# Optimization experiments

Measured on AMD Instinct MI355X. Metric: run time of the kernel, lower is better.

Reference implementation:

```python
import jax, jax.numpy as jnp
import numpy as np

DIM = 384
DEPTH = 4
HEADS = 6
DIM_HEAD = 64
INNER = HEADS * DIM_HEAD  # 384
MLP = 1536
B, N = 4, 2048


def setup_inputs() -> dict:
    key = jax.random.key(0)
    ks = jax.random.split(key, 7)
    s = 0.02
    x = jax.random.normal(ks[0], (B, N, DIM), dtype=jnp.float32)
    Wqkv = jax.random.normal(ks[1], (DEPTH, DIM, 3 * INNER), dtype=jnp.float32) * s
    Wout = jax.random.normal(ks[2], (DEPTH, INNER, DIM), dtype=jnp.float32) * s
    W1 = jax.random.normal(ks[3], (DEPTH, DIM, MLP), dtype=jnp.float32) * s
    b1 = jax.random.normal(ks[4], (DEPTH, MLP), dtype=jnp.float32) * s
    W2 = jax.random.normal(ks[5], (DEPTH, MLP, DIM), dtype=jnp.float32) * s
    b2 = jax.random.normal(ks[6], (DEPTH, DIM), dtype=jnp.float32) * s
    return {"x": x, "Wqkv": Wqkv, "Wout": Wout, "W1": W1, "b1": b1, "W2": W2, "b2": b2}


def _attention(x, Wqkv_l, Wout_l):
    scale = DIM_HEAD ** (-0.5)
    qkv = jnp.einsum('bnd,de->bne', x, Wqkv_l)  # [B,N,3*INNER]
    q, k, v = jnp.split(qkv, 3, axis=-1)
    # [B,N,INNER] -> [B,H,N,Dh]
    reshape = lambda t: t.reshape(B, N, HEADS, DIM_HEAD).transpose(0, 2, 1, 3)
    q, k, v = reshape(q), reshape(k), reshape(v)
    dots = jnp.einsum('bhnd,bhmd->bhnm', q, k) * scale
    attn = jax.nn.softmax(dots, axis=-1)
    out = jnp.einsum('bhnm,bhmd->bhnd', attn, v)
    out = out.transpose(0, 2, 1, 3).reshape(B, N, INNER)
    return jnp.einsum('bne,ed->bnd', out, Wout_l)


def _ff(x, W1_l, b1_l, W2_l, b2_l):
    h = jax.nn.gelu(jnp.einsum('bnd,dh->bnh', x, W1_l) + b1_l, approximate=False)
    return jnp.einsum('bnh,hd->bnd', h, W2_l) + b2_l


def reference(x, Wqkv, Wout, W1, b1, W2, b2):
    for l in range(DEPTH):
        x = _attention(x, Wqkv[l], Wout[l]) + x
        x = _ff(x, W1[l], b1[l], W2[l], b2[l]) + x
    return x
```

## Files before the change

### kernel.cpp

```cpp
#include <hip/hip_runtime.h>
#include <stdint.h>

#define HEADS 6
#define NN 2048
#define BB 4
#define MTOT (BB*NN)
#define DEPTH 4

typedef unsigned short u16;
typedef __attribute__((ext_vector_type(8))) short bf16x8;
typedef __attribute__((ext_vector_type(4))) float f32x4;
typedef __attribute__((ext_vector_type(16))) float f32x16;

#define MFMA32(a,b,c) __builtin_amdgcn_mfma_f32_32x32x16_bf16((a),(b),(c),0,0,0)

#define QSC 0.18033688011112042f

__device__ __forceinline__ u16 f2bf(float f) {
  union { float f; uint32_t u; } v; v.f = f;
  uint32_t r = v.u + 0x7fffu + ((v.u >> 16) & 1u);
  return (u16)(r >> 16);
}

__device__ __forceinline__ uint32_t pk2(float lo, float hi) {
  uint32_t r;
  asm("v_cvt_pk_bf16_f32 %0, %1, %2" : "=v"(r) : "v"(lo), "v"(hi));
  return r;
}

__device__ __forceinline__ void gload_lds16(const void* g, void* l) {
  __builtin_amdgcn_global_load_lds((const __attribute__((address_space(1))) void*)g,
                                   (__attribute__((address_space(3))) void*)l, 16, 0, 0);
}

__global__ __launch_bounds__(256)
void wtrans_k(const float* __restrict__ in, u16* __restrict__ out, int K, int N) {
  __shared__ float t[32][33];
  const int z = blockIdx.z;
  in  += (size_t)z * K * N;
  out += (size_t)z * K * N;
  const int n0 = blockIdx.x * 32, k0 = blockIdx.y * 32;
  const int tx = threadIdx.x & 31, ty = threadIdx.x >> 5;
#pragma unroll
  for (int i = 0; i < 4; ++i)
    t[ty + i*8][tx] = in[(size_t)(k0 + ty + i*8) * N + n0 + tx];
  __syncthreads();
#pragma unroll
  for (int i = 0; i < 4; ++i)
    out[(size_t)(n0 + ty + i*8) * K + k0 + tx] = f2bf(t[tx][ty + i*8]);
}

__global__ __launch_bounds__(256)
void xprep_k(const float* __restrict__ x, u16* __restrict__ xbf, int n) {
  int i = blockIdx.x * 256 + threadIdx.x;
  if (i < n) xbf[i] = f2bf(x[i]);
}

template<int MODE>
__global__ __launch_bounds__(256)
void gemm64_k(const u16* __restrict__ A, const u16* __restrict__ Bt,
              const float* __restrict__ bias, const float* __restrict__ res,
              float* __restrict__ outF, u16* __restrict__ outB,
              u16* __restrict__ qb, u16* __restrict__ kb, u16* __restrict__ vtb,
              int M, int N, int K) {
  __shared__ u16 smA[64 * 64];
  __shared__ u16 smB[64 * 64];
  const int tid = threadIdx.x;
  const int lane = tid & 63, wv = tid >> 6;
  const int wr = wv >> 1, wc = wv & 1;
  const int l31 = lane & 31, h2 = lane >> 5;
  const int row0 = blockIdx.y * 64, col0 = blockIdx.x * 64;

  f32x16 acc;
#pragma unroll
  for (int i = 0; i < 16; ++i) acc[i] = 0.f;

  const int c0 = tid, c1 = tid + 256;
  const int r0 = c0 >> 3, s0 = (c0 & 7) ^ (r0 & 7);
  const int r1 = c1 >> 3, s1 = (c1 & 7) ^ (r1 & 7);

  const int ksteps = K >> 6;
  for (int kt = 0; kt < ksteps; ++kt) {
    const int k0 = kt << 6;
    const u16* Ab = A  + (size_t)row0 * K + k0;
    const u16* Bb = Bt + (size_t)col0 * K + k0;
    gload_lds16(Ab + (size_t)r0 * K + s0 * 8, smA + wv * 512);
    gload_lds16(Ab + (size_t)r1 * K + s1 * 8, smA + 2048 + wv * 512);
    gload_lds16(Bb + (size_t)r0 * K + s0 * 8, smB + wv * 512);
    gload_lds16(Bb + (size_t)r1 * K + s1 * 8, smB + 2048 + wv * 512);
    __syncthreads();
    const int ra = wr * 32 + l31;
    const int rb = wc * 32 + l31;
#pragma unroll
    for (int ks = 0; ks < 4; ++ks) {
      bf16x8 af = *(const bf16x8*)(smA + ra * 64 + (((ks * 2 + h2) ^ (ra & 7)) * 8));
      bf16x8 bf = *(const bf16x8*)(smB + rb * 64 + (((ks * 2 + h2) ^ (rb & 7)) * 8));
      acc = MFMA32(af, bf, acc);
    }
    __syncthreads();
  }

  const int col = col0 + wc * 32 + l31;
  if (MODE == 0) {
    const int sec = col / 384, c3 = col - sec * 384;
    const int hh = c3 >> 6, d = c3 & 63;
#pragma unroll
    for (int c = 0; c < 4; ++c)
#pragma unroll
      for (int j = 0; j < 4; ++j) {
        const int row = row0 + wr * 32 + 8 * c + 4 * h2 + j;
        const int bb = row >> 11, n = row & 2047;
        const float v = acc[4 * c + j];
        if (sec == 0)       qb [(((size_t)bb * HEADS + hh) * NN + n) * 64 + d] = f2bf(v * QSC);
        else if (sec == 1)  kb [(((size_t)bb * HEADS + hh) * NN + n) * 64 + d] = f2bf(v);
        else                vtb[(((size_t)bb * HEADS + hh) * 64 + d) * NN + n] = f2bf(v);
      }
  } else {
#pragma unroll
    for (int c = 0; c < 4; ++c)
#pragma unroll
      for (int j = 0; j < 4; ++j) {
        const int row = row0 + wr * 32 + 8 * c + 4 * h2 + j;
        float v = acc[4 * c + j];
        if (MODE == 1) {
          size_t idx = (size_t)row * N + col;
          v += res[idx];
          outF[idx] = v;
          outB[idx] = f2bf(v);
        } else if (MODE == 2) {
          v += bias[col];
          v = 0.5f * v * (1.0f + erff(v * 0.70710678118f));
          outB[(size_t)row * N + col] = f2bf(v);
        } else {
          size_t idx = (size_t)row * N + col;
          v += bias[col] + res[idx];
          outF[idx] = v;
          outB[idx] = f2bf(v);
        }
      }
  }
}

__global__ __launch_bounds__(256)
void attn_k(const u16* __restrict__ qb, const u16* __restrict__ kb,
            const u16* __restrict__ vtb, u16* __restrict__ ob) {
  __shared__ u16 sall[4][4096];
  const int tid = threadIdx.x;
  const int lane = tid & 63, wv = tid >> 6;
  const int l31 = lane & 31, h2 = lane >> 5;
  const int hs = wv >> 1;
  const int qg = wv & 1;

  const int lid = blockIdx.y * 32 + blockIdx.x;
  const int xcd = lid & 7, ii = lid >> 3;
  const int bh = 3 * xcd + (ii >> 5);
  const int qblk = ii & 31;
  const int b = bh / HEADS, h = bh - b * HEADS;
  const int q0 = qblk * 64 + qg * 32;

  const u16* Qb = qb + ((size_t)bh * NN + q0 + l31) * 64;
  bf16x8 qf[4];
#pragma unroll
  for (int ct2 = 0; ct2 < 4; ++ct2)
    qf[ct2] = *(const bf16x8*)(Qb + ct2 * 16 + h2 * 8);

  float m = -1e30f, s = 0.f;
  f32x16 acc[2];
#pragma unroll
  for (int dg = 0; dg < 2; ++dg)
#pragma unroll
    for (int i = 0; i < 16; ++i) acc[dg][i] = 0.f;
  const f32x16 zero16 = {0.f,0.f,0.f,0.f,0.f,0.f,0.f,0.f,0.f,0.f,0.f,0.f,0.f,0.f,0.f,0.f};

  const u16* Kb0 = kb  + (size_t)bh * NN * 64;
  const u16* Vt0 = vtb + (size_t)bh * 64 * NN;
  const int rK = tid >> 3, sK = (tid & 7) ^ (rK & 7);
  const int rV = tid >> 2, sV = (tid & 3) ^ (rV & 3);

#define STAGE2(buf, t) do { \
    _Pragma("unroll") \
    for (int hf = 0; hf < 2; ++hf) { \
      gload_lds16(Kb0 + ((size_t)(hf * 1024 + (t) * 32 + rK)) * 64 + sK * 8, \
                  sall[buf] + hf * 2048 + wv * 512); \
      gload_lds16(Vt0 + (size_t)rV * NN + hf * 1024 + (t) * 32 + sV * 8, \
                  sall[2 + (buf)] + hf * 2048 + wv * 512); \
    } \
  } while (0)

  STAGE2(0, 0);
  __syncthreads();

  int cur = 0;
  const int NT = 1024 / 32;
  for (int kt = 0; kt < NT; ++kt) {
    if (kt + 1 < NT) STAGE2(cur ^ 1, kt + 1);
    const u16* kcur = sall[cur] + hs * 2048;
    const u16* vcur = sall[2 + cur] + hs * 2048;

    f32x16 st = zero16;
    {
      const u16* krow = kcur + l31 * 64;
#pragma unroll
      for (int ct2 = 0; ct2 < 4; ++ct2) {
        bf16x8 kf = *(const bf16x8*)(krow + (((ct2 * 2 + h2) ^ (l31 & 7)) * 8));
        st = MFMA32(kf, qf[ct2], st);
      }
    }

    float tmax = -1e30f;
#pragma unroll
    for (int i = 0; i < 16; ++i) tmax = fmaxf(tmax, st[i]);
    if (!__all(tmax <= m + 8.0f)) {
      float rm = fmaxf(tmax, __shfl_xor(tmax, 32));
      float mn = fmaxf(m, rm);
      float al = __builtin_amdgcn_exp2f(m - mn);
      s *= al;
#pragma unroll
      for (int dg = 0; dg < 2; ++dg)
#pragma unroll
        for (int i = 0; i < 16; ++i) acc[dg][i] *= al;
      m = mn;
    }
    float p[16];
    float r = 0.f;
#pragma unroll
    for (int i = 0; i < 16; ++i) {
      float t = __builtin_amdgcn_exp2f(st[i] - m);
      p[i] = t;
      r += t;
    }
    r += __shfl_xor(r, 32);
    s += r;

    bf16x8 pf[2];
#pragma unroll
    for (int sub = 0; sub < 2; ++sub) {
      const int s8 = sub * 8;
      uint32_t X0 = pk2(p[s8 + 0], p[s8 + 1]);
      uint32_t X1 = pk2(p[s8 + 2], p[s8 + 3]);
      uint32_t Y0 = pk2(p[s8 + 4], p[s8 + 5]);
      uint32_t Y1 = pk2(p[s8 + 6], p[s8 + 7]);
      asm volatile("v_permlane32_swap_b32 %0, %1" : "+v"(X0), "+v"(Y0));
      asm volatile("v_permlane32_swap_b32 %0, %1" : "+v"(X1), "+v"(Y1));
      union { uint32_t u[4]; bf16x8 v; } pu;
      pu.u[0] = X0; pu.u[1] = X1; pu.u[2] = Y0; pu.u[3] = Y1;
      pf[sub] = pu.v;
    }

#pragma unroll
    for (int ks = 0; ks < 2; ++ks)
#pragma unroll
      for (int dg = 0; dg < 2; ++dg) {
        const int d = dg * 32 + l31;
        bf16x8 vf = *(const bf16x8*)(vcur + d * 32 + (((ks * 2 + h2) ^ (d & 3)) * 8));
        acc[dg] = MFMA32(vf, pf[ks], acc[dg]);
      }

    __syncthreads();
    cur ^= 1;
  }

  float* mb = (float*)sall;
  if (wv >= 2) {
    const int base = ((wv - 2) * 64 + lane) * 36;
#pragma unroll
    for (int dg = 0; dg < 2; ++dg)
#pragma unroll
      for (int i = 0; i < 16; ++i) mb[base + dg * 16 + i] = acc[dg][i];
    mb[base + 32] = m;
    mb[base + 33] = s;
  }
  __syncthreads();
  if (wv < 2) {
    const int base = (wv * 64 + lane) * 36;
    const float m2 = mb[base + 32], s2 = mb[base + 33];
    const float M  = fmaxf(m, m2);
    const float a1 = __builtin_amdgcn_exp2f(m  - M);
    const float a2 = __builtin_amdgcn_exp2f(m2 - M);
    const float inv = 1.f / (s * a1 + s2 * a2);
    u16* orow = ob + ((size_t)b * NN + q0 + l31) * 384 + h * 64;
#pragma unroll
    for (int dg = 0; dg < 2; ++dg)
#pragma unroll
      for (int c = 0; c < 4; ++c) {
        float v0 = (acc[dg][4*c + 0] * a1 + mb[base + dg*16 + 4*c + 0] * a2) * inv;
        float v1 = (acc[dg][4*c + 1] * a1 + mb[base + dg*16 + 4*c + 1] * a2) * inv;
        float v2 = (acc[dg][4*c + 2] * a1 + mb[base + dg*16 + 4*c + 2] * a2) * inv;
        float v3 = (acc[dg][4*c + 3] * a1 + mb[base + dg*16 + 4*c + 3] * a2) * inv;
        uint2 w;
        w.x = pk2(v0, v1);
        w.y = pk2(v2, v3);
        *(uint2*)(orow + dg * 32 + 8 * c + 4 * h2) = w;
      }
  }
}

extern "C" void kernel_launch(void* const* d_in, const int* in_sizes, int n_in,
                              void* d_out, int out_size, void* d_ws, size_t ws_size,
                              hipStream_t stream) {
  (void)in_sizes; (void)n_in; (void)out_size; (void)ws_size;
  const float* x    = (const float*)d_in[0];
  const float* Wqkv = (const float*)d_in[1];
  const float* Wout = (const float*)d_in[2];
  const float* W1   = (const float*)d_in[3];
  const float* b1   = (const float*)d_in[4];
  const float* W2   = (const float*)d_in[5];
  const float* b2   = (const float*)d_in[6];
  float* out = (float*)d_out;

  char* ws = (char*)d_ws;
  size_t off = 0;
  auto alloc = [&](size_t bytes) { char* p = ws + off; off += (bytes + 255) & ~(size_t)255; return p; };
  u16*   wqkvT = (u16*)alloc((size_t)DEPTH * 1152 * 384 * 2);
  u16*   woutT = (u16*)alloc((size_t)DEPTH * 384 * 384 * 2);
  u16*   w1T   = (u16*)alloc((size_t)DEPTH * 1536 * 384 * 2);
  u16*   w2T   = (u16*)alloc((size_t)DEPTH * 384 * 1536 * 2);
  u16*   xbf   = (u16*)alloc((size_t)MTOT * 384 * 2);
  float* xres  = (float*)alloc((size_t)MTOT * 384 * 4);
  u16*   qbuf  = (u16*)alloc((size_t)MTOT * 384 * 2);
  u16*   kbuf  = (u16*)alloc((size_t)MTOT * 384 * 2);
  u16*   vtbuf = (u16*)alloc((size_t)MTOT * 384 * 2);
  u16*   obuf  = (u16*)alloc((size_t)MTOT * 384 * 2);
  u16*   hbuf  = (u16*)alloc((size_t)MTOT * 1536 * 2);

  wtrans_k<<<dim3(1152/32, 384/32, DEPTH), 256, 0, stream>>>(Wqkv, wqkvT, 384, 1152);
  wtrans_k<<<dim3( 384/32, 384/32, DEPTH), 256, 0, stream>>>(Wout, woutT, 384, 384);
  wtrans_k<<<dim3(1536/32, 384/32, DEPTH), 256, 0, stream>>>(W1,   w1T,   384, 1536);
  wtrans_k<<<dim3( 384/32,1536/32, DEPTH), 256, 0, stream>>>(W2,   w2T,   1536, 384);
  xprep_k<<<(MTOT*384 + 255)/256, 256, 0, stream>>>(x, xbf, MTOT*384);

  for (int l = 0; l < DEPTH; ++l) {
    gemm64_k<0><<<dim3(1152/64, MTOT/64), 256, 0, stream>>>(
        xbf, wqkvT + (size_t)l*1152*384, nullptr, nullptr, nullptr, nullptr,
        qbuf, kbuf, vtbuf, MTOT, 1152, 384);
    attn_k<<<dim3(32, 24), 256, 0, stream>>>(qbuf, kbuf, vtbuf, obuf);
    gemm64_k<1><<<dim3(384/64, MTOT/64), 256, 0, stream>>>(
        obuf, woutT + (size_t)l*384*384, nullptr, (l == 0 ? x : xres), xres, xbf,
        nullptr, nullptr, nullptr, MTOT, 384, 384);
    gemm64_k<2><<<dim3(1536/64, MTOT/64), 256, 0, stream>>>(
        xbf, w1T + (size_t)l*1536*384, b1 + l*1536, nullptr, nullptr, hbuf,
        nullptr, nullptr, nullptr, MTOT, 1536, 384);
    gemm64_k<3><<<dim3(384/64, MTOT/64), 256, 0, stream>>>(
        hbuf, w2T + (size_t)l*384*1536, b2 + l*384, xres,
        (l == DEPTH-1 ? out : xres), xbf,
        nullptr, nullptr, nullptr, MTOT, 384, 1536);
  }
}
```

Measured before the change: 555.7 us.

## Triple-buffer attention K/V loads and remap GEMM blocks across XCDs

The attention kernel moves from double to triple buffering of K/V tiles in LDS. It prefetches two tiles ahead and uses explicit vmcnt waits with raw barriers instead of __syncthreads, so more global-load latency overlaps with MFMA work. The GEMM kernel remaps block IDs so consecutive blocks on the same XCD cover contiguous tiles, to improve L2 locality. The costs are more LDS per block, which may lower occupancy, and the remap assumes the grid size is divisible by 8.

```diff
diff --git a/kernel.cpp b/kernel.cpp
--- a/kernel.cpp
+++ b/kernel.cpp
@@ -69,7 +69,12 @@
   const int lane = tid & 63, wv = tid >> 6;
   const int wr = wv >> 1, wc = wv & 1;
   const int l31 = lane & 31, h2 = lane >> 5;
-  const int row0 = blockIdx.y * 64, col0 = blockIdx.x * 64;
+
+  const int gx = gridDim.x;
+  const int lid = blockIdx.y * gx + blockIdx.x;
+  const int chunk = (gx * gridDim.y) >> 3;
+  const int v_ = (lid & 7) * chunk + (lid >> 3);
+  const int row0 = (v_ / gx) * 64, col0 = (v_ % gx) * 64;
 
   f32x16 acc;
 #pragma unroll
@@ -144,7 +149,8 @@
 __global__ __launch_bounds__(256)
 void attn_k(const u16* __restrict__ qb, const u16* __restrict__ kb,
             const u16* __restrict__ vtb, u16* __restrict__ ob) {
-  __shared__ u16 sall[4][4096];
+  __shared__ u16 kb3[3][2][32 * 64];
+  __shared__ u16 vb3[3][2][64 * 32];
   const int tid = threadIdx.x;
   const int lane = tid & 63, wv = tid >> 6;
   const int l31 = lane & 31, h2 = lane >> 5;
@@ -177,25 +183,33 @@
   const int rK = tid >> 3, sK = (tid & 7) ^ (rK & 7);
   const int rV = tid >> 2, sV = (tid & 3) ^ (rV & 3);
 
-#define STAGE2(buf, t) do { \
+  u16* kflat = &kb3[0][0][0];
+  u16* vflat = &vb3[0][0][0];
+
+#define STAGEB(bi, t) do { \
+    u16* kd_ = kflat + (bi) * 4096; \
+    u16* vd_ = vflat + (bi) * 4096; \
     _Pragma("unroll") \
     for (int hf = 0; hf < 2; ++hf) { \
       gload_lds16(Kb0 + ((size_t)(hf * 1024 + (t) * 32 + rK)) * 64 + sK * 8, \
-                  sall[buf] + hf * 2048 + wv * 512); \
+                  kd_ + hf * 2048 + wv * 512); \
       gload_lds16(Vt0 + (size_t)rV * NN + hf * 1024 + (t) * 32 + sV * 8, \
-                  sall[2 + (buf)] + hf * 2048 + wv * 512); \
+                  vd_ + hf * 2048 + wv * 512); \
     } \
   } while (0)
 
-  STAGE2(0, 0);
-  __syncthreads();
-
-  int cur = 0;
+  STAGEB(0, 0);
+  STAGEB(1, 1);
+  asm volatile("s_waitcnt vmcnt(4)" ::: "memory");
+  __builtin_amdgcn_s_barrier();
+  __builtin_amdgcn_sched_barrier(0);
+
   const int NT = 1024 / 32;
   for (int kt = 0; kt < NT; ++kt) {
-    if (kt + 1 < NT) STAGE2(cur ^ 1, kt + 1);
-    const u16* kcur = sall[cur] + hs * 2048;
-    const u16* vcur = sall[2 + cur] + hs * 2048;
+    const int cb = kt % 3;
+    if (kt + 2 < NT) STAGEB((kt + 2) % 3, kt + 2);
+    const u16* kcur = kflat + cb * 4096 + hs * 2048;
+    const u16* vcur = vflat + cb * 4096 + hs * 2048;
 
     f32x16 st = zero16;
     {
@@ -256,11 +270,13 @@
         acc[dg] = MFMA32(vf, pf[ks], acc[dg]);
       }
 
-    __syncthreads();
-    cur ^= 1;
-  }
-
-  float* mb = (float*)sall;
+    if (kt + 2 < NT) asm volatile("s_waitcnt vmcnt(4)" ::: "memory");
+    else             asm volatile("s_waitcnt vmcnt(0)" ::: "memory");
+    __builtin_amdgcn_s_barrier();
+    __builtin_amdgcn_sched_barrier(0);
+  }
+
+  float* mb = (float*)kb3;
   if (wv >= 2) {
     const int base = ((wv - 2) * 64 + lane) * 36;
 #pragma unroll
```

Result: faster. 525.0 us (-5.5%).
